# Optimization experiments

Measured on AMD Instinct MI355X. Metric: run time of the kernel, lower is better.

Reference implementation:

```python
import jax, jax.numpy as jnp
import numpy as np

D_MODEL = 1024


def setup_inputs() -> dict:
    key = jax.random.key(0)
    ks = jax.random.split(key, 9)
    B, S, D = 4, 2048, D_MODEL
    scale = 1.0 / np.sqrt(D)
    inp = {
        "tokens": jax.random.normal(ks[0], (B, S, D), dtype=jnp.float32),
        "Wq": jax.random.normal(ks[1], (D, D), dtype=jnp.float32) * scale,
        "bq": jnp.zeros((D,), dtype=jnp.float32),
        "Wk": jax.random.normal(ks[2], (D, D), dtype=jnp.float32) * scale,
        "bk": jnp.zeros((D,), dtype=jnp.float32),
        "Wv": jax.random.normal(ks[3], (D, D), dtype=jnp.float32) * scale,
        "bv": jnp.zeros((D,), dtype=jnp.float32),
        "Wo": jax.random.normal(ks[4], (D, D), dtype=jnp.float32) * scale,
        "bo": jnp.zeros((D,), dtype=jnp.float32),
    }
    return inp


def reference(tokens, Wq, bq, Wk, bk, Wv, bv, Wo, bo):
    # use_activation=True, use_residual=True
    residual = tokens
    x = jax.nn.gelu(tokens, approximate=False)  # F.gelu default is exact (erf)
    q = jnp.einsum("bsd,de->bse", x, Wq) + bq
    k = jnp.einsum("bsd,de->bse", x, Wk) + bk
    v = jnp.einsum("bsd,de->bse", x, Wv) + bv
    scale = 1.0 / jnp.sqrt(jnp.asarray(tokens.shape[-1], dtype=tokens.dtype))
    scores = jnp.einsum("bqd,bkd->bqk", q, k) * scale  # [B,S,S]
    attn = jax.nn.softmax(scores, axis=-1)
    mixed = jnp.einsum("bqk,bkd->bqd", attn, v)
    out = jnp.einsum("bsd,de->bse", mixed, Wo) + bo
    return out + residual
```

## Files before the change

### kernel.cpp

```cpp
#include <hip/hip_runtime.h>
#include <hip/hip_bf16.h>
#include <cstdint>
#include <cstddef>

typedef unsigned short u16;
using frag_ab = __attribute__((ext_vector_type(8))) short;
using f32x4   = __attribute__((ext_vector_type(4))) float;

__device__ __forceinline__ u16 f2bf(float x) {
    __hip_bfloat16 h = __float2bfloat16(x);
    return *reinterpret_cast<u16*>(&h);
}

__device__ __forceinline__ void gload_lds16(const u16* g, u16* l) {
    __builtin_amdgcn_global_load_lds(
        (const __attribute__((address_space(1))) uint32_t*)g,
        (__attribute__((address_space(3)))       uint32_t*)l,
        16, 0, 0);
}

#define WAITV4() do { asm volatile("s_waitcnt vmcnt(4)" ::: "memory"); \
                      __builtin_amdgcn_sched_barrier(0); } while (0)
#define BAR()    do { asm volatile("" ::: "memory"); __builtin_amdgcn_s_barrier(); \
                      __builtin_amdgcn_sched_barrier(0); } while (0)
#define LGKMC(N) do { asm volatile("s_waitcnt lgkmcnt(" #N ")" ::: "memory"); \
                      __builtin_amdgcn_sched_barrier(0); } while (0)
#define LGKM0()  LGKMC(0)

template<int EPI, int BN_>
__global__ __launch_bounds__(512, 2)
void gemm8p(const u16* __restrict__ A, const u16* __restrict__ Bt,
            void* __restrict__ C0,
            const float* __restrict__ b0, const float* __restrict__ resid,
            int K, int lda, int ldb, int ldc,
            long long sA, long long sB, long long sC, float alpha,
            float* __restrict__ partials)
{
    constexpr int NFQ    = BN_ / 64;
    constexpr int WN     = BN_ / 2;
    constexpr int BUFSTR = 16384 + BN_ * 64;
    __shared__ __align__(16) u16 lds[2 * BUFSTR];

    const int z = blockIdx.z;
    A  += (long long)z * sA;
    Bt += (long long)z * sB;

    const int gx  = gridDim.x;
    const int nwg = gx * gridDim.y;
    const int cpx = nwg >> 3;
    int lin = blockIdx.x + gx * blockIdx.y;
    lin = (lin & 7) * cpx + (lin >> 3);
    const int m0 = (lin / gx) * 256;
    const int n0 = (lin % gx) * BN_;

    const int t    = threadIdx.x;
    const int lane = t & 63;
    const int wave = t >> 6;
    const int wm   = wave >> 1;
    const int wn   = wave & 1;

    const int r0  = t >> 3;
    const int ssw = (t & 7) ^ (r0 & 7);
    const u16* gsA0_0 = A  + (size_t)(m0 +       r0) * lda + ssw * 8;
    const u16* gsA0_1 = A  + (size_t)(m0 +  64 + r0) * lda + ssw * 8;
    const u16* gsA1_0 = A  + (size_t)(m0 + 128 + r0) * lda + ssw * 8;
    const u16* gsA1_1 = A  + (size_t)(m0 + 192 + r0) * lda + ssw * 8;
    const u16* gsB0_0 = Bt + (size_t)(n0 +       r0) * ldb + ssw * 8;
    const u16* gsB0_1 = Bt + (size_t)(n0 +  64 + r0) * ldb + ssw * 8;
    const u16* gsB1_0 = (BN_ == 256) ? Bt + (size_t)(n0 + 128 + r0) * ldb + ssw * 8 : gsB0_0;
    const u16* gsB1_1 = (BN_ == 256) ? Bt + (size_t)(n0 + 192 + r0) * ldb + ssw * 8 : gsB0_1;

#define OPO_A 0
#define OPO_B 16384
#define STAGE(BI, OP, H, KT) do {                                              \
    gload_lds16(gs##OP##H##_0 + (size_t)(KT) * 64,                             \
                lds + (BI) * BUFSTR + OPO_##OP + (H) * 8192 + t * 8);          \
    gload_lds16(gs##OP##H##_1 + (size_t)(KT) * 64,                             \
                lds + (BI) * BUFSTR + OPO_##OP + (H) * 8192 + 4096 + t * 8);   \
} while (0)

    const int ar   = lane & 15;
    const int ko   = lane >> 4;
    const int aoff = (wm * 64 + ar) * 64;
    const int boff = OPO_B + (wn * WN + ar) * 64;
    const int as0  = ((0 + ko) ^ (ar & 7)) * 8;
    const int as1  = ((4 + ko) ^ (ar & 7)) * 8;

    frag_ab areg[2][2];
    frag_ab breg[2][NFQ][2];
    f32x4   acc[4][2 * NFQ] = {};

#define RDA(BI, MQ) do { _Pragma("unroll") for (int mf = 0; mf < 2; ++mf) {    \
    areg[mf][0] = *(const frag_ab*)(lds + (BI)*BUFSTR + aoff + ((MQ)*2+mf)*1024 + as0); \
    areg[mf][1] = *(const frag_ab*)(lds + (BI)*BUFSTR + aoff + ((MQ)*2+mf)*1024 + as1); } } while (0)

#define RDB(BI, NQ) do { _Pragma("unroll") for (int jf = 0; jf < NFQ; ++jf) {  \
    breg[NQ][jf][0] = *(const frag_ab*)(lds + (BI)*BUFSTR + boff + ((NQ)*NFQ+jf)*1024 + as0); \
    breg[NQ][jf][1] = *(const frag_ab*)(lds + (BI)*BUFSTR + boff + ((NQ)*NFQ+jf)*1024 + as1); } } while (0)

#define MMAQ(MQ, NQ) do { __builtin_amdgcn_s_setprio(1);                       \
    _Pragma("unroll") for (int mf = 0; mf < 2; ++mf)                           \
    _Pragma("unroll") for (int jf = 0; jf < NFQ; ++jf) {                       \
        acc[(MQ)*2+mf][(NQ)*NFQ+jf] = __builtin_amdgcn_mfma_f32_16x16x32_bf16( \
            areg[mf][0], breg[NQ][jf][0], acc[(MQ)*2+mf][(NQ)*NFQ+jf], 0,0,0); \
        acc[(MQ)*2+mf][(NQ)*NFQ+jf] = __builtin_amdgcn_mfma_f32_16x16x32_bf16( \
            areg[mf][1], breg[NQ][jf][1], acc[(MQ)*2+mf][(NQ)*NFQ+jf], 0,0,0); \
    } __builtin_amdgcn_s_setprio(0); } while (0)

    const int nk = K / 64;
    STAGE(0, A, 0, 0); STAGE(0, A, 1, 0); STAGE(0, B, 0, 0);
    if constexpr (BN_ == 256) STAGE(0, B, 1, 0);
    STAGE(1, B, 0, 1); STAGE(1, A, 0, 1);
    WAITV4();
    BAR();

    const int nIter = nk >> 1;
    for (int it = 0; it < nIter; ++it) {
        const int O  = 2 * it + 1;
        const int E2 = (2 * it + 2 < nk) ? 2 * it + 2 : nk - 1;
        const int O2 = (2 * it + 3 < nk) ? 2 * it + 3 : nk - 1;

        RDA(0, 0); RDB(0, 0);
        STAGE(1, A, 1, O);
        if constexpr (BN_ == 256) LGKMC(8);
        BAR(); LGKM0(); MMAQ(0, 0);
        RDB(0, 1);
        if constexpr (BN_ == 256) STAGE(1, B, 1, O);
        BAR(); LGKM0(); MMAQ(0, 1);
        RDA(0, 1);
        STAGE(0, B, 0, E2);
        BAR(); LGKM0(); MMAQ(1, 0);
        STAGE(0, A, 0, E2);
        WAITV4();
        BAR(); MMAQ(1, 1);
        RDA(1, 0); RDB(1, 0);
        STAGE(0, A, 1, E2);
        if constexpr (BN_ == 256) LGKMC(8);
        BAR(); LGKM0(); MMAQ(0, 0);
        RDB(1, 1);
        if constexpr (BN_ == 256) STAGE(0, B, 1, E2);
        BAR(); LGKM0(); MMAQ(0, 1);
        RDA(1, 1);
        STAGE(1, B, 0, O2);
        BAR(); LGKM0(); MMAQ(1, 0);
        STAGE(1, A, 0, O2);
        WAITV4();
        BAR(); MMAQ(1, 1);
    }

    const int cr = (lane >> 4) * 4;
    const int cc = lane & 15;

    float rs[4][4];
    if constexpr (EPI == 1) {
        #pragma unroll
        for (int mi = 0; mi < 4; ++mi)
            #pragma unroll
            for (int r = 0; r < 4; ++r) rs[mi][r] = 0.0f;
    }

    #pragma unroll
    for (int mi = 0; mi < 4; ++mi) {
        const int rowb = m0 + wm * 64 + mi * 16 + cr;
        #pragma unroll
        for (int gj = 0; gj < 2 * NFQ; ++gj) {
            const int col = n0 + wn * WN + gj * 16 + cc;
            const float bvv = (EPI == 3) ? b0[col] : 0.0f;
            #pragma unroll
            for (int r = 0; r < 4; ++r) {
                const size_t row = (size_t)(rowb + r);
                float v = acc[mi][gj][r];
                if (EPI == 1) { v = __expf(v * alpha); rs[mi][r] += v; }
                if (EPI == 2) v *= b0[(size_t)z * 2048 + row];
                v += bvv;
                if (EPI == 3) {
                    v += resid[row * ldc + col];
                    ((float*)C0)[(size_t)z * sC + row * ldc + col] = v;
                } else {
                    ((u16*)C0)[(size_t)z * sC + row * ldc + col] = f2bf(v);
                }
            }
        }
    }

    if constexpr (EPI == 1) {
        #pragma unroll
        for (int mi = 0; mi < 4; ++mi)
            #pragma unroll
            for (int r = 0; r < 4; ++r) {
                float s = rs[mi][r];
                s += __shfl_xor(s, 1); s += __shfl_xor(s, 2);
                s += __shfl_xor(s, 4); s += __shfl_xor(s, 8);
                rs[mi][r] = s;
            }
        if (cc == 0) {
            const int chunk = (n0 >> 7) + wn;
            #pragma unroll
            for (int mi = 0; mi < 4; ++mi) {
                const int rowb = m0 + wm * 64 + mi * 16 + cr;
                #pragma unroll
                for (int r = 0; r < 4; ++r)
                    partials[((size_t)z * 2048 + rowb + r) * 16 + chunk] = rs[mi][r];
            }
        }
    }
#undef STAGE
#undef RDA
#undef RDB
#undef MMAQ
#undef OPO_A
#undef OPO_B
}

__global__ __launch_bounds__(256, 2)
void gemm128_qkv(const u16* __restrict__ A, const u16* __restrict__ Bt,
                 void* __restrict__ C0, void* __restrict__ C1, void* __restrict__ C2,
                 const float* __restrict__ b0, const float* __restrict__ b1,
                 const float* __restrict__ b2,
                 int K, int lda, int ldb, int ldc)
{
    constexpr int BUFSTR = 16384;
    __shared__ __align__(16) u16 lds[2 * BUFSTR];

    const int gx  = gridDim.x;
    const int nwg = gx * gridDim.y;
    const int cpx = nwg >> 3;
    int lin = blockIdx.x + gx * blockIdx.y;
    lin = (lin & 7) * cpx + (lin >> 3);
    const int m0 = (lin / gx) * 128;
    const int n0 = (lin % gx) * 128;

    const int t    = threadIdx.x;
    const int lane = t & 63;
    const int wave = t >> 6;
    const int wm   = wave >> 1;
    const int wn   = wave & 1;

    const int r0  = t >> 3;
    const int ssw = (t & 7) ^ (r0 & 7);
    const u16* gsA0_0 = A  + (size_t)(m0 +       r0) * lda + ssw * 8;
    const u16* gsA0_1 = A  + (size_t)(m0 +  32 + r0) * lda + ssw * 8;
    const u16* gsA1_0 = A  + (size_t)(m0 +  64 + r0) * lda + ssw * 8;
    const u16* gsA1_1 = A  + (size_t)(m0 +  96 + r0) * lda + ssw * 8;
    const u16* gsB0_0 = Bt + (size_t)(n0 +       r0) * ldb + ssw * 8;
    const u16* gsB0_1 = Bt + (size_t)(n0 +  32 + r0) * ldb + ssw * 8;
    const u16* gsB1_0 = Bt + (size_t)(n0 +  64 + r0) * ldb + ssw * 8;
    const u16* gsB1_1 = Bt + (size_t)(n0 +  96 + r0) * ldb + ssw * 8;

#define OPO_A 0
#define OPO_B 8192
#define STAGE(BI, OP, H, KT) do {                                              \
    gload_lds16(gs##OP##H##_0 + (size_t)(KT) * 64,                             \
                lds + (BI) * BUFSTR + OPO_##OP + (H) * 4096 + t * 8);          \
    gload_lds16(gs##OP##H##_1 + (size_t)(KT) * 64,                             \
                lds + (BI) * BUFSTR + OPO_##OP + (H) * 4096 + 2048 + t * 8);   \
} while (0)

    const int ar   = lane & 15;
    const int ko   = lane >> 4;
    const int aoff = (wm * 64 + ar) * 64;
    const int boff = OPO_B + (wn * 64 + ar) * 64;
    const int as0  = ((0 + ko) ^ (ar & 7)) * 8;
    const int as1  = ((4 + ko) ^ (ar & 7)) * 8;

    frag_ab areg[2][2];
    frag_ab breg[2][2][2];
    f32x4   acc[4][4] = {};

#define RDA(BI, MQ) do { _Pragma("unroll") for (int mf = 0; mf < 2; ++mf) {    \
    areg[mf][0] = *(const frag_ab*)(lds + (BI)*BUFSTR + aoff + ((MQ)*2+mf)*1024 + as0); \
    areg[mf][1] = *(const frag_ab*)(lds + (BI)*BUFSTR + aoff + ((MQ)*2+mf)*1024 + as1); } } while (0)

#define RDB(BI, NQ) do { _Pragma("unroll") for (int jf = 0; jf < 2; ++jf) {    \
    breg[NQ][jf][0] = *(const frag_ab*)(lds + (BI)*BUFSTR + boff + ((NQ)*2+jf)*1024 + as0); \
    breg[NQ][jf][1] = *(const frag_ab*)(lds + (BI)*BUFSTR + boff + ((NQ)*2+jf)*1024 + as1); } } while (0)

#define MMAQ(MQ, NQ) do { __builtin_amdgcn_s_setprio(1);                       \
    _Pragma("unroll") for (int mf = 0; mf < 2; ++mf)                           \
    _Pragma("unroll") for (int jf = 0; jf < 2; ++jf) {                         \
        acc[(MQ)*2+mf][(NQ)*2+jf] = __builtin_amdgcn_mfma_f32_16x16x32_bf16(   \
            areg[mf][0], breg[NQ][jf][0], acc[(MQ)*2+mf][(NQ)*2+jf], 0,0,0);   \
        acc[(MQ)*2+mf][(NQ)*2+jf] = __builtin_amdgcn_mfma_f32_16x16x32_bf16(   \
            areg[mf][1], breg[NQ][jf][1], acc[(MQ)*2+mf][(NQ)*2+jf], 0,0,0);   \
    } __builtin_amdgcn_s_setprio(0); } while (0)

    const int nk = K / 64;
    STAGE(0, A, 0, 0); STAGE(0, A, 1, 0); STAGE(0, B, 0, 0); STAGE(0, B, 1, 0);
    STAGE(1, B, 0, 1); STAGE(1, A, 0, 1);
    WAITV4();
    BAR();

    const int nIter = nk >> 1;
    for (int it = 0; it < nIter; ++it) {
        const int O  = 2 * it + 1;
        const int E2 = (2 * it + 2 < nk) ? 2 * it + 2 : nk - 1;
        const int O2 = (2 * it + 3 < nk) ? 2 * it + 3 : nk - 1;

        RDA(0, 0); RDB(0, 0); STAGE(1, A, 1, O);  BAR(); LGKM0(); MMAQ(0, 0);
        RDB(0, 1);            STAGE(1, B, 1, O);  BAR(); LGKM0(); MMAQ(0, 1);
        RDA(0, 1);            STAGE(0, B, 0, E2); BAR(); LGKM0(); MMAQ(1, 0);
        STAGE(0, A, 0, E2);   WAITV4();           BAR();          MMAQ(1, 1);
        RDA(1, 0); RDB(1, 0); STAGE(0, A, 1, E2); BAR(); LGKM0(); MMAQ(0, 0);
        RDB(1, 1);            STAGE(0, B, 1, E2); BAR(); LGKM0(); MMAQ(0, 1);
        RDA(1, 1);            STAGE(1, B, 0, O2); BAR(); LGKM0(); MMAQ(1, 0);
        STAGE(1, A, 0, O2);   WAITV4();           BAR();          MMAQ(1, 1);
    }

    const int cr = (lane >> 4) * 4;
    const int cc = lane & 15;

    const int plane = n0 >> 10;
    void*        Cw = (plane == 0) ? C0 : (plane == 1) ? C1 : C2;
    const float* bw = (plane == 0) ? b0 : (plane == 1) ? b1 : b2;
    const int    nc = n0 & 1023;

    #pragma unroll
    for (int mi = 0; mi < 4; ++mi) {
        const int rowb = m0 + wm * 64 + mi * 16 + cr;
        #pragma unroll
        for (int gj = 0; gj < 4; ++gj) {
            const int col = nc + wn * 64 + gj * 16 + cc;
            const float bvv = bw[col];
            #pragma unroll
            for (int r = 0; r < 4; ++r) {
                const size_t row = (size_t)(rowb + r);
                ((u16*)Cw)[row * ldc + col] = f2bf(acc[mi][gj][r] + bvv);
            }
        }
    }
#undef STAGE
#undef RDA
#undef RDB
#undef MMAQ
#undef OPO_A
#undef OPO_B
}

__global__ __launch_bounds__(256)
void gelu_to_bf16(const float4* __restrict__ in, uint2* __restrict__ outp)
{
    const int i = blockIdx.x * 256 + threadIdx.x;
    float4 x = in[i];
    auto g = [](float v) { return 0.5f * v * (1.0f + erff(v * 0.70710678118654752f)); };
    union { u16 u[4]; uint2 q; } pk;
    pk.u[0] = f2bf(g(x.x));
    pk.u[1] = f2bf(g(x.y));
    pk.u[2] = f2bf(g(x.z));
    pk.u[3] = f2bf(g(x.w));
    outp[i] = pk.q;
}

__global__ void wtrans_kernel(const float* __restrict__ W0, const float* __restrict__ W1,
                              const float* __restrict__ W2, const float* __restrict__ W3,
                              u16* __restrict__ WT, int D)
{
    __shared__ float tile[32][33];
    const float* W = (blockIdx.z == 0) ? W0 : (blockIdx.z == 1) ? W1 : (blockIdx.z == 2) ? W2 : W3;
    u16* o = WT + (size_t)blockIdx.z * D * D;
    const int n0 = blockIdx.x * 32, k0 = blockIdx.y * 32;
    const int tx = threadIdx.x, ty = threadIdx.y;
    tile[ty][tx] = W[(size_t)(k0 + ty) * D + n0 + tx];
    __syncthreads();
    o[(size_t)(n0 + ty) * D + k0 + tx] = f2bf(tile[tx][ty]);
}

__global__ void vtrans_kernel(const u16* __restrict__ v, u16* __restrict__ vt, int S, int D)
{
    __shared__ u16 tile[32][34];
    const u16* vb = v + (size_t)blockIdx.z * S * D;
    u16* ob = vt + (size_t)blockIdx.z * D * S;
    const int d0 = blockIdx.x * 32, s0 = blockIdx.y * 32;
    const int tx = threadIdx.x, ty = threadIdx.y;
    tile[ty][tx] = vb[(size_t)(s0 + ty) * D + d0 + tx];
    __syncthreads();
    ob[(size_t)(d0 + ty) * S + s0 + tx] = tile[tx][ty];
}

__global__ __launch_bounds__(256)
void invl_kernel(const float* __restrict__ partials, float* __restrict__ invl)
{
    const int r = blockIdx.x * 256 + threadIdx.x;
    const float* p = partials + (size_t)r * 16;
    float s = 0.0f;
    #pragma unroll
    for (int i = 0; i < 16; ++i) s += p[i];
    invl[r] = 1.0f / s;
}

extern "C" void kernel_launch(void* const* d_in, const int* in_sizes, int n_in,
                              void* d_out, int out_size, void* d_ws, size_t ws_size,
                              hipStream_t stream)
{
    const int B = 4, S = 2048, D = 1024;
    const int M = B * S;

    const float* tokens = (const float*)d_in[0];
    const float* Wq = (const float*)d_in[1];
    const float* bq = (const float*)d_in[2];
    const float* Wk = (const float*)d_in[3];
    const float* bk = (const float*)d_in[4];
    const float* Wv = (const float*)d_in[5];
    const float* bv = (const float*)d_in[6];
    const float* Wo = (const float*)d_in[7];
    const float* bo = (const float*)d_in[8];
    float* out = (float*)d_out;

    char* ws = (char*)d_ws;
    size_t o = 0;
    u16* x_bf = (u16*)(ws + o); o += (size_t)M * D * 2;
    u16* wT   = (u16*)(ws + o); o += (size_t)4 * D * D * 2;
    u16* q_bf = (u16*)(ws + o); o += (size_t)M * D * 2;
    u16* k_bf = (u16*)(ws + o); o += (size_t)M * D * 2;
    u16* v_bf = (u16*)(ws + o); o += (size_t)M * D * 2;
    u16*   E        = (u16*)(ws + o);   o += (size_t)B * S * S * 2;
    float* partials = (float*)(ws + o); o += (size_t)B * S * 16 * 4;
    float* invl     = (float*)(ws + o); o += (size_t)B * S * 4;
    u16* vt    = q_bf;
    u16* mixed = x_bf;

    gelu_to_bf16<<<dim3(M * D / 4 / 256), dim3(256), 0, stream>>>(
        (const float4*)tokens, (uint2*)x_bf);

    wtrans_kernel<<<dim3(D / 32, D / 32, 4), dim3(32, 32), 0, stream>>>(Wq, Wk, Wv, Wo, wT, D);

    gemm128_qkv<<<dim3(3 * D / 128, M / 128, 1), dim3(256), 0, stream>>>(
        x_bf, wT, q_bf, k_bf, v_bf, bq, bk, bv, D, D, D, D);

    gemm8p<1, 256><<<dim3(S / 256, S / 256, B), dim3(512), 0, stream>>>(
        q_bf, k_bf, E, nullptr, nullptr,
        D, D, D, S, (long long)S * D, (long long)S * D, (long long)S * S, 0.03125f,
        partials);

    vtrans_kernel<<<dim3(D / 32, S / 32, B), dim3(32, 32), 0, stream>>>(v_bf, vt, S, D);

    invl_kernel<<<dim3(B * S / 256), dim3(256), 0, stream>>>(partials, invl);

    gemm8p<2, 128><<<dim3(D / 128, S / 256, B), dim3(512), 0, stream>>>(
        E, vt, mixed, invl, nullptr,
        S, S, S, D, (long long)S * S, (long long)D * S, (long long)S * D, 1.0f, nullptr);

    gemm8p<3, 128><<<dim3(D / 128, M / 256, 1), dim3(512), 0, stream>>>(
        mixed, wT + 3 * D * D, out, bo, tokens,
        D, D, D, D, 0, 0, 0, 1.0f, nullptr);
}
```

Before: 192.7 us.

## Fuse V transpose, softmax normalizer and prep kernels into neighboring kernels

The QKV GEMM epilogue now writes V already transposed through an LDS staging tile, so the separate V transpose kernel goes away. The PV GEMM computes the inverse softmax row sums from the partials in its own epilogue, replacing the separate invl kernel. GELU conversion and weight transposition are merged into one prep launch, and each transpose block now handles 4 rows per thread. Together these cut kernel launches and an intermediate round-trip of V through global memory, in exchange for extra LDS work and barriers in the GEMM epilogues.

```diff
diff --git a/kernel.cpp b/kernel.cpp
--- a/kernel.cpp
+++ b/kernel.cpp
@@ -20,6 +20,8 @@
 }
 
 #define WAITV4() do { asm volatile("s_waitcnt vmcnt(4)" ::: "memory"); \
+                      __builtin_amdgcn_sched_barrier(0); } while (0)
+#define WAITV0() do { asm volatile("s_waitcnt vmcnt(0)" ::: "memory"); \
                       __builtin_amdgcn_sched_barrier(0); } while (0)
 #define BAR()    do { asm volatile("" ::: "memory"); __builtin_amdgcn_s_barrier(); \
                       __builtin_amdgcn_sched_barrier(0); } while (0)
@@ -151,6 +153,20 @@
     const int cr = (lane >> 4) * 4;
     const int cc = lane & 15;
 
+    float* fl = (float*)lds;
+    if constexpr (EPI == 2) {
+        WAITV0();
+        BAR();
+        if (t < 256) {
+            const float* p = partials + ((size_t)z * 2048 + m0 + t) * 16;
+            float s = 0.0f;
+            #pragma unroll
+            for (int i = 0; i < 16; ++i) s += p[i];
+            fl[t] = 1.0f / s;
+        }
+        BAR();
+    }
+
     float rs[4][4];
     if constexpr (EPI == 1) {
         #pragma unroll
@@ -162,6 +178,7 @@
     #pragma unroll
     for (int mi = 0; mi < 4; ++mi) {
         const int rowb = m0 + wm * 64 + mi * 16 + cr;
+        const int rloc = wm * 64 + mi * 16 + cr;
         #pragma unroll
         for (int gj = 0; gj < 2 * NFQ; ++gj) {
             const int col = n0 + wn * WN + gj * 16 + cc;
@@ -171,7 +188,7 @@
                 const size_t row = (size_t)(rowb + r);
                 float v = acc[mi][gj][r];
                 if (EPI == 1) { v = __expf(v * alpha); rs[mi][r] += v; }
-                if (EPI == 2) v *= b0[(size_t)z * 2048 + row];
+                if (EPI == 2) v *= fl[rloc + r];
                 v += bvv;
                 if (EPI == 3) {
                     v += resid[row * ldc + col];
@@ -310,21 +327,51 @@
     const int cc = lane & 15;
 
     const int plane = n0 >> 10;
-    void*        Cw = (plane == 0) ? C0 : (plane == 1) ? C1 : C2;
-    const float* bw = (plane == 0) ? b0 : (plane == 1) ? b1 : b2;
-    const int    nc = n0 & 1023;
-
-    #pragma unroll
-    for (int mi = 0; mi < 4; ++mi) {
-        const int rowb = m0 + wm * 64 + mi * 16 + cr;
-        #pragma unroll
-        for (int gj = 0; gj < 4; ++gj) {
-            const int col = nc + wn * 64 + gj * 16 + cc;
-            const float bvv = bw[col];
-            #pragma unroll
-            for (int r = 0; r < 4; ++r) {
-                const size_t row = (size_t)(rowb + r);
-                ((u16*)Cw)[row * ldc + col] = f2bf(acc[mi][gj][r] + bvv);
+    const int nc    = n0 & 1023;
+
+    if (plane == 2) {
+        WAITV0();
+        BAR();
+        constexpr int TP = 136;
+        u16* T = lds;
+        #pragma unroll
+        for (int mi = 0; mi < 4; ++mi) {
+            const int rloc = wm * 64 + mi * 16 + cr;
+            #pragma unroll
+            for (int gj = 0; gj < 4; ++gj) {
+                const int cl = wn * 64 + gj * 16 + cc;
+                const float bvv = b2[nc + cl];
+                #pragma unroll
+                for (int r = 0; r < 4; ++r)
+                    T[cl * TP + rloc + r] = f2bf(acc[mi][gj][r] + bvv);
+            }
+        }
+        BAR();
+        const int bb   = m0 >> 11;
+        const int s0   = m0 & 2047;
+        const int d    = t >> 1;
+        const int half = t & 1;
+        const u16* src = T + d * TP + half * 64;
+        u16* dg = (u16*)C2 + (size_t)bb * 1024 * 2048
+                + (size_t)(nc + d) * 2048 + s0 + half * 64;
+        #pragma unroll
+        for (int j = 0; j < 8; ++j)
+            ((uint4*)dg)[j] = ((const uint4*)src)[j];
+    } else {
+        void*        Cw = (plane == 0) ? C0 : C1;
+        const float* bw = (plane == 0) ? b0 : b1;
+        #pragma unroll
+        for (int mi = 0; mi < 4; ++mi) {
+            const int rowb = m0 + wm * 64 + mi * 16 + cr;
+            #pragma unroll
+            for (int gj = 0; gj < 4; ++gj) {
+                const int col = nc + wn * 64 + gj * 16 + cc;
+                const float bvv = bw[col];
+                #pragma unroll
+                for (int r = 0; r < 4; ++r) {
+                    const size_t row = (size_t)(rowb + r);
+                    ((u16*)Cw)[row * ldc + col] = f2bf(acc[mi][gj][r] + bvv);
+                }
             }
         }
     }
@@ -337,54 +384,41 @@
 }
 
 __global__ __launch_bounds__(256)
-void gelu_to_bf16(const float4* __restrict__ in, uint2* __restrict__ outp)
-{
-    const int i = blockIdx.x * 256 + threadIdx.x;
-    float4 x = in[i];
-    auto g = [](float v) { return 0.5f * v * (1.0f + erff(v * 0.70710678118654752f)); };
-    union { u16 u[4]; uint2 q; } pk;
-    pk.u[0] = f2bf(g(x.x));
-    pk.u[1] = f2bf(g(x.y));
-    pk.u[2] = f2bf(g(x.z));
-    pk.u[3] = f2bf(g(x.w));
-    outp[i] = pk.q;
-}
-
-__global__ void wtrans_kernel(const float* __restrict__ W0, const float* __restrict__ W1,
-                              const float* __restrict__ W2, const float* __restrict__ W3,
-                              u16* __restrict__ WT, int D)
+void prep_kernel(const float4* __restrict__ in, uint2* __restrict__ outp,
+                 const float* __restrict__ W0, const float* __restrict__ W1,
+                 const float* __restrict__ W2, const float* __restrict__ W3,
+                 u16* __restrict__ WT, int D, int NG)
 {
     __shared__ float tile[32][33];
-    const float* W = (blockIdx.z == 0) ? W0 : (blockIdx.z == 1) ? W1 : (blockIdx.z == 2) ? W2 : W3;
-    u16* o = WT + (size_t)blockIdx.z * D * D;
-    const int n0 = blockIdx.x * 32, k0 = blockIdx.y * 32;
-    const int tx = threadIdx.x, ty = threadIdx.y;
-    tile[ty][tx] = W[(size_t)(k0 + ty) * D + n0 + tx];
+    const int b = blockIdx.x;
+    const int t = threadIdx.x;
+    if (b < NG) {
+        const int i = b * 256 + t;
+        float4 x = in[i];
+        auto g = [](float v) { return 0.5f * v * (1.0f + erff(v * 0.70710678118654752f)); };
+        union { u16 u[4]; uint2 q; } pk;
+        pk.u[0] = f2bf(g(x.x));
+        pk.u[1] = f2bf(g(x.y));
+        pk.u[2] = f2bf(g(x.z));
+        pk.u[3] = f2bf(g(x.w));
+        outp[i] = pk.q;
+        return;
+    }
+    const int j   = b - NG;
+    const int z   = j >> 10;
+    const int rem = j & 1023;
+    const int n0  = (rem & 31) * 32;
+    const int k0  = (rem >> 5) * 32;
+    const float* W = (z == 0) ? W0 : (z == 1) ? W1 : (z == 2) ? W2 : W3;
+    u16* o = WT + (size_t)z * D * D;
+    const int tx = t & 31, ty = t >> 5;
+    #pragma unroll
+    for (int r = 0; r < 4; ++r)
+        tile[ty + 8 * r][tx] = W[(size_t)(k0 + ty + 8 * r) * D + n0 + tx];
     __syncthreads();
-    o[(size_t)(n0 + ty) * D + k0 + tx] = f2bf(tile[tx][ty]);
-}
-
-__global__ void vtrans_kernel(const u16* __restrict__ v, u16* __restrict__ vt, int S, int D)
-{
-    __shared__ u16 tile[32][34];
-    const u16* vb = v + (size_t)blockIdx.z * S * D;
-    u16* ob = vt + (size_t)blockIdx.z * D * S;
-    const int d0 = blockIdx.x * 32, s0 = blockIdx.y * 32;
-    const int tx = threadIdx.x, ty = threadIdx.y;
-    tile[ty][tx] = vb[(size_t)(s0 + ty) * D + d0 + tx];
-    __syncthreads();
-    ob[(size_t)(d0 + ty) * S + s0 + tx] = tile[tx][ty];
-}
-
-__global__ __launch_bounds__(256)
-void invl_kernel(const float* __restrict__ partials, float* __restrict__ invl)
-{
-    const int r = blockIdx.x * 256 + threadIdx.x;
-    const float* p = partials + (size_t)r * 16;
-    float s = 0.0f;
     #pragma unroll
-    for (int i = 0; i < 16; ++i) s += p[i];
-    invl[r] = 1.0f / s;
+    for (int r = 0; r < 4; ++r)
+        o[(size_t)(n0 + ty + 8 * r) * D + k0 + tx] = f2bf(tile[tx][ty + 8 * r]);
 }
 
 extern "C" void kernel_launch(void* const* d_in, const int* in_sizes, int n_in,
@@ -411,33 +445,27 @@
     u16* wT   = (u16*)(ws + o); o += (size_t)4 * D * D * 2;
     u16* q_bf = (u16*)(ws + o); o += (size_t)M * D * 2;
     u16* k_bf = (u16*)(ws + o); o += (size_t)M * D * 2;
-    u16* v_bf = (u16*)(ws + o); o += (size_t)M * D * 2;
+    u16* vt   = (u16*)(ws + o); o += (size_t)M * D * 2;
     u16*   E        = (u16*)(ws + o);   o += (size_t)B * S * S * 2;
     float* partials = (float*)(ws + o); o += (size_t)B * S * 16 * 4;
-    float* invl     = (float*)(ws + o); o += (size_t)B * S * 4;
-    u16* vt    = q_bf;
     u16* mixed = x_bf;
 
-    gelu_to_bf16<<<dim3(M * D / 4 / 256), dim3(256), 0, stream>>>(
-        (const float4*)tokens, (uint2*)x_bf);
-
-    wtrans_kernel<<<dim3(D / 32, D / 32, 4), dim3(32, 32), 0, stream>>>(Wq, Wk, Wv, Wo, wT, D);
+    const int NG = M * D / 4 / 256;
+    prep_kernel<<<dim3(NG + 4096), dim3(256), 0, stream>>>(
+        (const float4*)tokens, (uint2*)x_bf, Wq, Wk, Wv, Wo, wT, D, NG);
 
     gemm128_qkv<<<dim3(3 * D / 128, M / 128, 1), dim3(256), 0, stream>>>(
-        x_bf, wT, q_bf, k_bf, v_bf, bq, bk, bv, D, D, D, D);
+        x_bf, wT, q_bf, k_bf, vt, bq, bk, bv, D, D, D, D);
 
     gemm8p<1, 256><<<dim3(S / 256, S / 256, B), dim3(512), 0, stream>>>(
         q_bf, k_bf, E, nullptr, nullptr,
         D, D, D, S, (long long)S * D, (long long)S * D, (long long)S * S, 0.03125f,
         partials);
 
-    vtrans_kernel<<<dim3(D / 32, S / 32, B), dim3(32, 32), 0, stream>>>(v_bf, vt, S, D);
-
-    invl_kernel<<<dim3(B * S / 256), dim3(256), 0, stream>>>(partials, invl);
-
     gemm8p<2, 128><<<dim3(D / 128, S / 256, B), dim3(512), 0, stream>>>(
-        E, vt, mixed, invl, nullptr,
-        S, S, S, D, (long long)S * S, (long long)D * S, (long long)S * D, 1.0f, nullptr);
+        E, vt, mixed, nullptr, nullptr,
+        S, S, S, D, (long long)S * S, (long long)D * S, (long long)S * D, 1.0f,
+        partials);
 
     gemm8p<3, 128><<<dim3(D / 128, M / 256, 1), dim3(512), 0, stream>>>(
         mixed, wT + 3 * D * D, out, bo, tokens,
```

Measured after the change: 172.7 us. 1.12x faster.
